# Kernel tuning notes

Measured on AMD Instinct MI355X. Metric: run time of the kernel, lower is better.

The kernel has to match this reference:

```python
import jax, jax.numpy as jnp
import numpy as np

B, D, H, W = 64, 64, 32, 32
K = 1024  # num_embeddings


def setup_inputs() -> dict:
    key = jax.random.key(0)
    kx, ke = jax.random.split(key)
    x = jax.random.normal(kx, (B, D, H, W), dtype=jnp.float32)
    # original init: uniform(-sqrt(3), sqrt(3)); randn is fine numerically, but
    # we match the original init distribution for fidelity
    limit = 3.0 ** 0.5
    embedding_table = jax.random.uniform(ke, (D, K), dtype=jnp.float32,
                                         minval=-limit, maxval=limit)
    return {"x": x, "embedding_table": embedding_table}


def reference(x, embedding_table):
    b, d, h, w = x.shape
    flat_x = x.transpose(0, 2, 3, 1).reshape(-1, d)            # [N, D]
    distances = ((flat_x ** 2).sum(1, keepdims=True)
                 - 2.0 * flat_x @ embedding_table
                 + (embedding_table ** 2).sum(0, keepdims=True))  # [N, K]
    encoding_indices = jnp.argmin(distances, axis=1)            # [N]
    quantized = embedding_table.T[encoding_indices]             # [N, D] gather
    quantized = quantized.reshape(b, h, w, d).transpose(0, 3, 1, 2)  # [B,D,H,W]
    dictionary_loss = jnp.mean((jax.lax.stop_gradient(x) - quantized) ** 2)
    commitment_loss = jnp.mean((x - jax.lax.stop_gradient(quantized)) ** 2)
    quantized_st = x + jax.lax.stop_gradient(quantized - x)     # straight-through
    return (quantized_st, dictionary_loss, commitment_loss,
            encoding_indices.reshape(b, -1))
```

## Files before the change

kernel.cpp:

```cpp
#include <hip/hip_runtime.h>


#define DDIM 64
#define KNUM 1024
#define HWN  1024
#define EPSS 0.01f

typedef __attribute__((ext_vector_type(8))) short short8v;
typedef __attribute__((ext_vector_type(4))) float f32x4;

__device__ __forceinline__ unsigned short bf16_rn(float v) {
    unsigned u = __float_as_uint(v);
    return (unsigned short)((u + 0x7FFFu + ((u >> 16) & 1u)) >> 16);
}
__device__ __forceinline__ float bf16f(unsigned short h) {
    return __uint_as_float(((unsigned)h) << 16);
}

__global__ __launch_bounds__(256) void vq_convert_e(const float* __restrict__ E,
                                                    float* __restrict__ esq,
                                                    unsigned short* __restrict__ eh,
                                                    unsigned short* __restrict__ el) {
    int k = blockIdx.x * 256 + threadIdx.x;
    float s = 0.f;
    #pragma unroll 8
    for (int d = 0; d < DDIM; ++d) {
        float v = E[d * KNUM + k];
        s = fmaf(v, v, s);
        unsigned short h = bf16_rn(v);
        float lo = v - bf16f(h);
        eh[k * DDIM + d] = h;
        el[k * DDIM + d] = bf16_rn(lo);
    }
    esq[k] = s;
}

__global__ __launch_bounds__(256, 4) void vq_mfma_fused(const float* __restrict__ x,
                                                        const float* __restrict__ E,
                                                        const unsigned short* __restrict__ eh,
                                                        const unsigned short* __restrict__ el,
                                                        const float* __restrict__ esq,
                                                        float* __restrict__ oidx,
                                                        float* __restrict__ out_q,
                                                        float* __restrict__ partial) {
    __shared__ unsigned short blds[2][8192];
    __shared__ float esqlds[KNUM];
    __shared__ int   klds[64];
    __shared__ float redlds[4];

    const int t = threadIdx.x;
    const int wv = t >> 6, l = t & 63;
    const int m = l & 15, g = l >> 4;
    const int tile = blockIdx.x * 4 + wv;
    const int n0 = blockIdx.x * 64;
    const int b  = n0 >> 10, hw0 = n0 & 1023;

    __builtin_amdgcn_global_load_lds(
        (const __attribute__((address_space(1))) void*)(esq + t * 4),
        (__attribute__((address_space(3))) void*)&esqlds[t * 4], 16, 0, 0);

    const int sr   = t >> 3;
    const int sc   = (t & 7) * 16;
    const int scsw = sc ^ ((sr & 7) << 4);
    const unsigned short* srcrow0 =
        (sr < 16) ? (eh + (size_t)sr * DDIM + (scsw >> 1))
                  : (el + (size_t)(sr - 16) * DDIM + (scsw >> 1));
    #define STAGEPH(BUF, P)                                                                  \
        _Pragma("unroll")                                                                    \
        for (int q = 0; q < 4; ++q)                                                          \
            __builtin_amdgcn_global_load_lds(                                                \
                (const __attribute__((address_space(1))) void*)(srcrow0 + (size_t)((P) * 4 + q) * 16 * DDIM), \
                (__attribute__((address_space(3))) void*)&blds[BUF][q * 2048 + t * 8],       \
                16, 0, 0);

    short8v axh[2], axl[2];
    {
        const int tn0 = tile * 16;
        const int tb = tn0 >> 10, thw = tn0 & 1023;
        const float* xg = x + (size_t)tb * (DDIM * HWN) + thw + m;
        #pragma unroll
        for (int s = 0; s < 2; ++s) {
            #pragma unroll
            for (int i = 0; i < 8; ++i) {
                float v = xg[(s * 32 + g * 8 + i) * HWN];
                unsigned short h = bf16_rn(v);
                axh[s][i] = (short)h;
                axl[s][i] = (short)bf16_rn(v - bf16f(h));
            }
        }
    }

    const int off_h0 = (m * 128 + (((g * 16)     ) ^ ((m & 7) << 4))) >> 1;
    const int off_h1 = (m * 128 + (((64 + g * 16)) ^ ((m & 7) << 4))) >> 1;
    const int off_l0 = off_h0 + 1024;
    const int off_l1 = off_h1 + 1024;

    float max1[4], max2[4]; int bk[4];
    #pragma unroll
    for (int j = 0; j < 4; ++j) { max1[j] = -3.4e38f; max2[j] = -3.4e38f; bk[j] = 0; }

    STAGEPH(0, 0);
    __syncthreads();

    for (int p = 0; p < 16; ++p) {
        const int cur = p & 1;
        if (p < 15) STAGEPH(cur ^ 1, p + 1);

        #pragma unroll
        for (int ktl = 0; ktl < 4; ++ktl) {
            const int kt = p * 4 + ktl;
            const unsigned short* bb = &blds[cur][ktl * 2048];
            const short8v bh0 = *reinterpret_cast<const short8v*>(bb + off_h0);
            const short8v bh1 = *reinterpret_cast<const short8v*>(bb + off_h1);
            const short8v bl0 = *reinterpret_cast<const short8v*>(bb + off_l0);
            const short8v bl1 = *reinterpret_cast<const short8v*>(bb + off_l1);
            const float ci = -0.5f * esqlds[kt * 16 + m];
            const f32x4 cinit = {ci, ci, ci, ci};

            f32x4 acc;
            acc = __builtin_amdgcn_mfma_f32_16x16x32_bf16(axh[0], bh0, cinit, 0, 0, 0);
            acc = __builtin_amdgcn_mfma_f32_16x16x32_bf16(axh[1], bh1, acc,  0, 0, 0);
            acc = __builtin_amdgcn_mfma_f32_16x16x32_bf16(axh[0], bl0, acc,  0, 0, 0);
            acc = __builtin_amdgcn_mfma_f32_16x16x32_bf16(axh[1], bl1, acc,  0, 0, 0);
            acc = __builtin_amdgcn_mfma_f32_16x16x32_bf16(axl[0], bh0, acc,  0, 0, 0);
            acc = __builtin_amdgcn_mfma_f32_16x16x32_bf16(axl[1], bh1, acc,  0, 0, 0);

            const int kcur = kt * 16 + m;
            #pragma unroll
            for (int j = 0; j < 4; ++j) {
                float s = acc[j];
                max2[j] = fmaxf(fminf(s, max1[j]), max2[j]);
                bool gt = s > max1[j];
                bk[j]   = gt ? kcur : bk[j];
                max1[j] = fmaxf(max1[j], s);
            }
        }
        __syncthreads();
    }
    #undef STAGEPH

    float* xlds = reinterpret_cast<float*>(&blds[0][0]);
    {
        const float* xbase = x + (size_t)b * (DDIM * HWN) + hw0;
        #pragma unroll
        for (int it = 0; it < 4; ++it) {
            int dbase = it * 16 + wv * 4;
            int dsub  = l >> 4;
            int off   = (l & 15) * 4;
            const float* gp = xbase + (dbase + dsub) * HWN + off;
            __builtin_amdgcn_global_load_lds(
                (const __attribute__((address_space(1))) void*)gp,
                (__attribute__((address_space(3))) void*)&xlds[dbase * 64 + l * 4],
                16, 0, 0);
        }
    }

    #pragma unroll
    for (int j = 0; j < 4; ++j) {
        float m1 = max1[j], m2 = max2[j]; int k1 = bk[j];
        #pragma unroll
        for (int off = 8; off >= 1; off >>= 1) {
            float om1 = __shfl_xor(m1, off, 16);
            float om2 = __shfl_xor(m2, off, 16);
            int   ok1 = __shfl_xor(k1, off, 16);
            if (om1 > m1 || (om1 == m1 && ok1 < k1)) {
                m2 = fmaxf(m1, om2); m1 = om1; k1 = ok1;
            } else {
                m2 = fmaxf(m2, (om1 == m1) ? om2 : om1);
            }
        }
        if (m == j) {
            int r = wv * 16 + g * 4 + j;
            klds[r] = (m1 - m2 < EPSS) ? -(k1 + 1) : k1;
        }
    }
    __syncthreads();

    for (int r = wv; r < 64; r += 4) {
        if (klds[r] >= 0) continue;
        float acc[16];
        #pragma unroll
        for (int kk = 0; kk < 16; ++kk) acc[kk] = 0.f;
        for (int d = 0; d < DDIM; ++d) {
            float xd = xlds[d * 64 + r];
            #pragma unroll
            for (int kk = 0; kk < 16; ++kk)
                acc[kk] = fmaf(xd, E[d * KNUM + kk * 64 + l], acc[kk]);
        }
        float bm = 3.4e38f; int bkk = KNUM;
        #pragma unroll
        for (int kk = 0; kk < 16; ++kk) {
            int k = kk * 64 + l;
            float dist = fmaf(-2.f, acc[kk], esqlds[k]);
            if (dist < bm) { bm = dist; bkk = k; }
        }
        #pragma unroll
        for (int off = 32; off >= 1; off >>= 1) {
            float ob = __shfl_xor(bm, off);
            int   ok = __shfl_xor(bkk, off);
            if (ob < bm || (ob == bm && ok < bkk)) { bm = ob; bkk = ok; }
        }
        if (l == 0) klds[r] = bkk;
    }
    __syncthreads();

    float lsum = 0.f;
    float* outbase = out_q + (size_t)b * (DDIM * HWN) + hw0;
    #pragma unroll 4
    for (int it = 0; it < 16; ++it) {
        int d = it * 4 + (t >> 6);
        int r = t & 63;
        int k = klds[r];
        float q  = E[d * KNUM + k];
        float xv = xlds[d * 64 + r];
        float diff = xv - q;
        lsum = fmaf(diff, diff, lsum);
        outbase[d * HWN + r] = q;
    }
    if (t < 64) oidx[n0 + t] = (float)klds[t];

    #pragma unroll
    for (int off = 32; off >= 1; off >>= 1)
        lsum += __shfl_xor(lsum, off);
    if ((t & 63) == 0) redlds[t >> 6] = lsum;
    __syncthreads();
    if (t == 0)
        partial[blockIdx.x] = (redlds[0] + redlds[1]) + (redlds[2] + redlds[3]);
}

__global__ __launch_bounds__(256) void vq_loss_kernel(const float* __restrict__ partial,
                                                      float* __restrict__ out_loss) {
    __shared__ float red[4];
    int t = threadIdx.x;
    float s = 0.f;
    #pragma unroll
    for (int it = 0; it < 4; ++it) s += partial[it * 256 + t];
    #pragma unroll
    for (int off = 32; off >= 1; off >>= 1) s += __shfl_xor(s, off);
    if ((t & 63) == 0) red[t >> 6] = s;
    __syncthreads();
    if (t == 0) {
        float loss = ((red[0] + red[1]) + (red[2] + red[3])) / 4194304.f;
        out_loss[0] = loss;
        out_loss[1] = loss;
    }
}

extern "C" void kernel_launch(void* const* d_in, const int* in_sizes, int n_in,
                              void* d_out, int out_size, void* d_ws, size_t ws_size,
                              hipStream_t stream) {
    const float* x = (const float*)d_in[0];
    const float* E = (const float*)d_in[1];
    float* out      = (float*)d_out;
    float* out_q    = out;
    float* out_loss = out + 4194304;
    float* oidx     = out + 4194306;

    float* esq     = (float*)d_ws;
    float* partial = esq + 1024;
    unsigned short* eh = (unsigned short*)(partial + 1024);
    unsigned short* el = eh + KNUM * DDIM;

    vq_convert_e<<<4, 256, 0, stream>>>(E, esq, eh, el);
    vq_mfma_fused<<<1024, 256, 0, stream>>>(x, E, eh, el, esq, oidx, out_q, partial);
    vq_loss_kernel<<<1, 256, 0, stream>>>(partial, out_loss);
}
```

Before: 64.07 us.

## Process two row tiles per wave to reuse staged codebook fragments

Each wave now computes two 16-row tiles against every staged codebook fragment, so a block covers 128 rows and the grid halves to 512 blocks. The LDS staging buffer doubles so each phase loads 8 k-tiles, halving the number of barrier phases. This cuts the codebook LDS traffic per row and the number of LDS reads per MFMA. The -0.5 scaling of the squared norms moves into the conversion kernel. In exchange it uses more registers and LDS, launch bounds drop to 2 blocks per CU, and fewer blocks means less parallelism across CUs.

Result: slower. 66.85 us (+4.3%).

```diff
diff --git a/kernel.cpp b/kernel.cpp
--- a/kernel.cpp
+++ b/kernel.cpp
@@ -18,7 +18,7 @@
 }
 
 __global__ __launch_bounds__(256) void vq_convert_e(const float* __restrict__ E,
-                                                    float* __restrict__ esq,
+                                                    float* __restrict__ esqm,
                                                     unsigned short* __restrict__ eh,
                                                     unsigned short* __restrict__ el) {
     int k = blockIdx.x * 256 + threadIdx.x;
@@ -32,32 +32,32 @@
         eh[k * DDIM + d] = h;
         el[k * DDIM + d] = bf16_rn(lo);
     }
-    esq[k] = s;
-}
-
-__global__ __launch_bounds__(256, 4) void vq_mfma_fused(const float* __restrict__ x,
+    esqm[k] = -0.5f * s;
+}
+
+__global__ __launch_bounds__(256, 2) void vq_mfma_fused(const float* __restrict__ x,
                                                         const float* __restrict__ E,
                                                         const unsigned short* __restrict__ eh,
                                                         const unsigned short* __restrict__ el,
-                                                        const float* __restrict__ esq,
+                                                        const float* __restrict__ esqm,
                                                         float* __restrict__ oidx,
                                                         float* __restrict__ out_q,
                                                         float* __restrict__ partial) {
-    __shared__ unsigned short blds[2][8192];
-    __shared__ float esqlds[KNUM];
-    __shared__ int   klds[64];
+    __shared__ unsigned short blds[2][16384];
+    __shared__ float esqmlds[KNUM];
+    __shared__ int   klds[128];
     __shared__ float redlds[4];
 
     const int t = threadIdx.x;
     const int wv = t >> 6, l = t & 63;
     const int m = l & 15, g = l >> 4;
-    const int tile = blockIdx.x * 4 + wv;
-    const int n0 = blockIdx.x * 64;
+    const int tileBase = blockIdx.x * 8 + wv * 2;
+    const int n0 = blockIdx.x * 128;
     const int b  = n0 >> 10, hw0 = n0 & 1023;
 
     __builtin_amdgcn_global_load_lds(
-        (const __attribute__((address_space(1))) void*)(esq + t * 4),
-        (__attribute__((address_space(3))) void*)&esqlds[t * 4], 16, 0, 0);
+        (const __attribute__((address_space(1))) void*)(esqm + t * 4),
+        (__attribute__((address_space(3))) void*)&esqmlds[t * 4], 16, 0, 0);
 
     const int sr   = t >> 3;
     const int sc   = (t & 7) * 16;
@@ -67,15 +67,16 @@
                   : (el + (size_t)(sr - 16) * DDIM + (scsw >> 1));
     #define STAGEPH(BUF, P)                                                                  \
         _Pragma("unroll")                                                                    \
-        for (int q = 0; q < 4; ++q)                                                          \
+        for (int q = 0; q < 8; ++q)                                                          \
             __builtin_amdgcn_global_load_lds(                                                \
-                (const __attribute__((address_space(1))) void*)(srcrow0 + (size_t)((P) * 4 + q) * 16 * DDIM), \
+                (const __attribute__((address_space(1))) void*)(srcrow0 + (size_t)((P) * 8 + q) * 16 * DDIM), \
                 (__attribute__((address_space(3))) void*)&blds[BUF][q * 2048 + t * 8],       \
                 16, 0, 0);
 
-    short8v axh[2], axl[2];
-    {
-        const int tn0 = tile * 16;
+    short8v axh[2][2], axl[2][2];
+    #pragma unroll
+    for (int T = 0; T < 2; ++T) {
+        const int tn0 = (tileBase + T) * 16;
         const int tb = tn0 >> 10, thw = tn0 & 1023;
         const float* xg = x + (size_t)tb * (DDIM * HWN) + thw + m;
         #pragma unroll
@@ -84,8 +85,8 @@
             for (int i = 0; i < 8; ++i) {
                 float v = xg[(s * 32 + g * 8 + i) * HWN];
                 unsigned short h = bf16_rn(v);
-                axh[s][i] = (short)h;
-                axl[s][i] = (short)bf16_rn(v - bf16f(h));
+                axh[T][s][i] = (short)h;
+                axl[T][s][i] = (short)bf16_rn(v - bf16f(h));
             }
         }
     }
@@ -95,44 +96,48 @@
     const int off_l0 = off_h0 + 1024;
     const int off_l1 = off_h1 + 1024;
 
-    float max1[4], max2[4]; int bk[4];
-    #pragma unroll
-    for (int j = 0; j < 4; ++j) { max1[j] = -3.4e38f; max2[j] = -3.4e38f; bk[j] = 0; }
+    float max1[2][4], max2[2][4]; int bk[2][4];
+    #pragma unroll
+    for (int T = 0; T < 2; ++T)
+        #pragma unroll
+        for (int j = 0; j < 4; ++j) { max1[T][j] = -3.4e38f; max2[T][j] = -3.4e38f; bk[T][j] = 0; }
 
     STAGEPH(0, 0);
     __syncthreads();
 
-    for (int p = 0; p < 16; ++p) {
+    for (int p = 0; p < 8; ++p) {
         const int cur = p & 1;
-        if (p < 15) STAGEPH(cur ^ 1, p + 1);
-
-        #pragma unroll
-        for (int ktl = 0; ktl < 4; ++ktl) {
-            const int kt = p * 4 + ktl;
+        if (p < 7) STAGEPH(cur ^ 1, p + 1);
+
+        #pragma unroll
+        for (int ktl = 0; ktl < 8; ++ktl) {
+            const int kt = p * 8 + ktl;
             const unsigned short* bb = &blds[cur][ktl * 2048];
             const short8v bh0 = *reinterpret_cast<const short8v*>(bb + off_h0);
             const short8v bh1 = *reinterpret_cast<const short8v*>(bb + off_h1);
             const short8v bl0 = *reinterpret_cast<const short8v*>(bb + off_l0);
             const short8v bl1 = *reinterpret_cast<const short8v*>(bb + off_l1);
-            const float ci = -0.5f * esqlds[kt * 16 + m];
+            const float ci = esqmlds[kt * 16 + m];
             const f32x4 cinit = {ci, ci, ci, ci};
-
-            f32x4 acc;
-            acc = __builtin_amdgcn_mfma_f32_16x16x32_bf16(axh[0], bh0, cinit, 0, 0, 0);
-            acc = __builtin_amdgcn_mfma_f32_16x16x32_bf16(axh[1], bh1, acc,  0, 0, 0);
-            acc = __builtin_amdgcn_mfma_f32_16x16x32_bf16(axh[0], bl0, acc,  0, 0, 0);
-            acc = __builtin_amdgcn_mfma_f32_16x16x32_bf16(axh[1], bl1, acc,  0, 0, 0);
-            acc = __builtin_amdgcn_mfma_f32_16x16x32_bf16(axl[0], bh0, acc,  0, 0, 0);
-            acc = __builtin_amdgcn_mfma_f32_16x16x32_bf16(axl[1], bh1, acc,  0, 0, 0);
-
             const int kcur = kt * 16 + m;
-            #pragma unroll
-            for (int j = 0; j < 4; ++j) {
-                float s = acc[j];
-                max2[j] = fmaxf(fminf(s, max1[j]), max2[j]);
-                bool gt = s > max1[j];
-                bk[j]   = gt ? kcur : bk[j];
-                max1[j] = fmaxf(max1[j], s);
+
+            #pragma unroll
+            for (int T = 0; T < 2; ++T) {
+                f32x4 acc;
+                acc = __builtin_amdgcn_mfma_f32_16x16x32_bf16(axh[T][0], bh0, cinit, 0, 0, 0);
+                acc = __builtin_amdgcn_mfma_f32_16x16x32_bf16(axh[T][1], bh1, acc,  0, 0, 0);
+                acc = __builtin_amdgcn_mfma_f32_16x16x32_bf16(axh[T][0], bl0, acc,  0, 0, 0);
+                acc = __builtin_amdgcn_mfma_f32_16x16x32_bf16(axh[T][1], bl1, acc,  0, 0, 0);
+                acc = __builtin_amdgcn_mfma_f32_16x16x32_bf16(axl[T][0], bh0, acc,  0, 0, 0);
+                acc = __builtin_amdgcn_mfma_f32_16x16x32_bf16(axl[T][1], bh1, acc,  0, 0, 0);
+                #pragma unroll
+                for (int j = 0; j < 4; ++j) {
+                    float s = acc[j];
+                    max2[T][j] = fmaxf(fminf(s, max1[T][j]), max2[T][j]);
+                    bool gt = s > max1[T][j];
+                    bk[T][j]   = gt ? kcur : bk[T][j];
+                    max1[T][j] = fmaxf(max1[T][j], s);
+                }
             }
         }
         __syncthreads();
@@ -143,62 +148,63 @@
     {
         const float* xbase = x + (size_t)b * (DDIM * HWN) + hw0;
         #pragma unroll
-        for (int it = 0; it < 4; ++it) {
-            int dbase = it * 16 + wv * 4;
-            int dsub  = l >> 4;
-            int off   = (l & 15) * 4;
-            const float* gp = xbase + (dbase + dsub) * HWN + off;
+        for (int it = 0; it < 8; ++it) {
+            int d   = it * 8 + (t >> 5);
+            int off = (t & 31) * 4;
+            const float* gp = xbase + d * HWN + off;
             __builtin_amdgcn_global_load_lds(
                 (const __attribute__((address_space(1))) void*)gp,
-                (__attribute__((address_space(3))) void*)&xlds[dbase * 64 + l * 4],
+                (__attribute__((address_space(3))) void*)&xlds[d * 128 + off],
                 16, 0, 0);
         }
     }
 
     #pragma unroll
-    for (int j = 0; j < 4; ++j) {
-        float m1 = max1[j], m2 = max2[j]; int k1 = bk[j];
-        #pragma unroll
-        for (int off = 8; off >= 1; off >>= 1) {
-            float om1 = __shfl_xor(m1, off, 16);
-            float om2 = __shfl_xor(m2, off, 16);
-            int   ok1 = __shfl_xor(k1, off, 16);
-            if (om1 > m1 || (om1 == m1 && ok1 < k1)) {
-                m2 = fmaxf(m1, om2); m1 = om1; k1 = ok1;
-            } else {
-                m2 = fmaxf(m2, (om1 == m1) ? om2 : om1);
-            }
-        }
-        if (m == j) {
-            int r = wv * 16 + g * 4 + j;
-            klds[r] = (m1 - m2 < EPSS) ? -(k1 + 1) : k1;
-        }
-    }
-    __syncthreads();
-
-    for (int r = wv; r < 64; r += 4) {
+    for (int T = 0; T < 2; ++T)
+        #pragma unroll
+        for (int j = 0; j < 4; ++j) {
+            float m1 = max1[T][j], m2 = max2[T][j]; int k1 = bk[T][j];
+            #pragma unroll
+            for (int off = 8; off >= 1; off >>= 1) {
+                float om1 = __shfl_xor(m1, off, 16);
+                float om2 = __shfl_xor(m2, off, 16);
+                int   ok1 = __shfl_xor(k1, off, 16);
+                if (om1 > m1 || (om1 == m1 && ok1 < k1)) {
+                    m2 = fmaxf(m1, om2); m1 = om1; k1 = ok1;
+                } else {
+                    m2 = fmaxf(m2, (om1 == m1) ? om2 : om1);
+                }
+            }
+            if (m == j) {
+                int r = (wv * 2 + T) * 16 + g * 4 + j;
+                klds[r] = (m1 - m2 < EPSS) ? -(k1 + 1) : k1;
+            }
+        }
+    __syncthreads();
+
+    for (int r = wv; r < 128; r += 4) {
         if (klds[r] >= 0) continue;
         float acc[16];
         #pragma unroll
         for (int kk = 0; kk < 16; ++kk) acc[kk] = 0.f;
         for (int d = 0; d < DDIM; ++d) {
-            float xd = xlds[d * 64 + r];
+            float xd = xlds[d * 128 + r];
             #pragma unroll
             for (int kk = 0; kk < 16; ++kk)
                 acc[kk] = fmaf(xd, E[d * KNUM + kk * 64 + l], acc[kk]);
         }
-        float bm = 3.4e38f; int bkk = KNUM;
+        float bm = -3.4e38f; int bkk = KNUM;
         #pragma unroll
         for (int kk = 0; kk < 16; ++kk) {
             int k = kk * 64 + l;
-            float dist = fmaf(-2.f, acc[kk], esqlds[k]);
-            if (dist < bm) { bm = dist; bkk = k; }
+            float sc = acc[kk] + esqmlds[k];
+            if (sc > bm) { bm = sc; bkk = k; }
         }
         #pragma unroll
         for (int off = 32; off >= 1; off >>= 1) {
             float ob = __shfl_xor(bm, off);
             int   ok = __shfl_xor(bkk, off);
-            if (ob < bm || (ob == bm && ok < bkk)) { bm = ob; bkk = ok; }
+            if (ob > bm || (ob == bm && ok < bkk)) { bm = ob; bkk = ok; }
         }
         if (l == 0) klds[r] = bkk;
     }
@@ -207,17 +213,18 @@
     float lsum = 0.f;
     float* outbase = out_q + (size_t)b * (DDIM * HWN) + hw0;
     #pragma unroll 4
-    for (int it = 0; it < 16; ++it) {
-        int d = it * 4 + (t >> 6);
-        int r = t & 63;
+    for (int it = 0; it < 32; ++it) {
+        int flat = it * 256 + t;
+        int d = flat >> 7;
+        int r = flat & 127;
         int k = klds[r];
         float q  = E[d * KNUM + k];
-        float xv = xlds[d * 64 + r];
+        float xv = xlds[d * 128 + r];
         float diff = xv - q;
         lsum = fmaf(diff, diff, lsum);
         outbase[d * HWN + r] = q;
     }
-    if (t < 64) oidx[n0 + t] = (float)klds[t];
+    if (t < 128) oidx[n0 + t] = (float)klds[t];
 
     #pragma unroll
     for (int off = 32; off >= 1; off >>= 1)
@@ -234,7 +241,7 @@
     int t = threadIdx.x;
     float s = 0.f;
     #pragma unroll
-    for (int it = 0; it < 4; ++it) s += partial[it * 256 + t];
+    for (int it = 0; it < 2; ++it) s += partial[it * 256 + t];
     #pragma unroll
     for (int off = 32; off >= 1; off >>= 1) s += __shfl_xor(s, off);
     if ((t & 63) == 0) red[t >> 6] = s;
@@ -256,12 +263,12 @@
     float* out_loss = out + 4194304;
     float* oidx     = out + 4194306;
 
-    float* esq     = (float*)d_ws;
-    float* partial = esq + 1024;
+    float* esqm    = (float*)d_ws;
+    float* partial = esqm + 1024;
     unsigned short* eh = (unsigned short*)(partial + 1024);
     unsigned short* el = eh + KNUM * DDIM;
 
-    vq_convert_e<<<4, 256, 0, stream>>>(E, esq, eh, el);
-    vq_mfma_fused<<<1024, 256, 0, stream>>>(x, E, eh, el, esq, oidx, out_q, partial);
+    vq_convert_e<<<4, 256, 0, stream>>>(E, esqm, eh, el);
+    vq_mfma_fused<<<512, 256, 0, stream>>>(x, E, eh, el, esqm, oidx, out_q, partial);
     vq_loss_kernel<<<1, 256, 0, stream>>>(partial, out_loss);
 }
```

## Split MFMA chain into independent accumulators and restructure LDS double-buffer sync

Applied to the files above, without the earlier changes.

The serial 6-MFMA dependency chain is replaced by three independent accumulator chains that are summed afterwards, which shortens MFMA latency stalls. The -0.5*|e|^2 term is precomputed in the conversion kernel, and the exact rescoring pass is rewritten to maximize that score instead of minimizing distance. The per-stage __syncthreads is replaced by explicit s_barrier plus vmcnt waits, so the prefetch of the next stage can stay in flight. The runner-up tracking in the shuffle reduction is also simplified, which slightly changes the near-tie detection and adds a few extra adds per tile.

Result: slower. 67.42 us (+5.2%).

```diff
diff --git a/kernel.cpp b/kernel.cpp
--- a/kernel.cpp
+++ b/kernel.cpp
@@ -9,6 +9,9 @@
 typedef __attribute__((ext_vector_type(8))) short short8v;
 typedef __attribute__((ext_vector_type(4))) float f32x4;
 
+#define VMWAIT(N) do { asm volatile("s_waitcnt vmcnt(" #N ")" ::: "memory"); \
+                       __builtin_amdgcn_sched_barrier(0); } while (0)
+
 __device__ __forceinline__ unsigned short bf16_rn(float v) {
     unsigned u = __float_as_uint(v);
     return (unsigned short)((u + 0x7FFFu + ((u >> 16) & 1u)) >> 16);
@@ -18,7 +21,7 @@
 }
 
 __global__ __launch_bounds__(256) void vq_convert_e(const float* __restrict__ E,
-                                                    float* __restrict__ esq,
+                                                    float* __restrict__ esqm,
                                                     unsigned short* __restrict__ eh,
                                                     unsigned short* __restrict__ el) {
     int k = blockIdx.x * 256 + threadIdx.x;
@@ -32,19 +35,19 @@
         eh[k * DDIM + d] = h;
         el[k * DDIM + d] = bf16_rn(lo);
     }
-    esq[k] = s;
+    esqm[k] = -0.5f * s;
 }
 
 __global__ __launch_bounds__(256, 4) void vq_mfma_fused(const float* __restrict__ x,
                                                         const float* __restrict__ E,
                                                         const unsigned short* __restrict__ eh,
                                                         const unsigned short* __restrict__ el,
-                                                        const float* __restrict__ esq,
+                                                        const float* __restrict__ esqm,
                                                         float* __restrict__ oidx,
                                                         float* __restrict__ out_q,
                                                         float* __restrict__ partial) {
     __shared__ unsigned short blds[2][8192];
-    __shared__ float esqlds[KNUM];
+    __shared__ float esqmlds[KNUM];
     __shared__ int   klds[64];
     __shared__ float redlds[4];
 
@@ -56,8 +59,8 @@
     const int b  = n0 >> 10, hw0 = n0 & 1023;
 
     __builtin_amdgcn_global_load_lds(
-        (const __attribute__((address_space(1))) void*)(esq + t * 4),
-        (__attribute__((address_space(3))) void*)&esqlds[t * 4], 16, 0, 0);
+        (const __attribute__((address_space(1))) void*)(esqm + t * 4),
+        (__attribute__((address_space(3))) void*)&esqmlds[t * 4], 16, 0, 0);
 
     const int sr   = t >> 3;
     const int sc   = (t & 7) * 16;
@@ -99,12 +102,16 @@
     #pragma unroll
     for (int j = 0; j < 4; ++j) { max1[j] = -3.4e38f; max2[j] = -3.4e38f; bk[j] = 0; }
 
+    const f32x4 zf = {0.f, 0.f, 0.f, 0.f};
+
     STAGEPH(0, 0);
-    __syncthreads();
 
     for (int p = 0; p < 16; ++p) {
         const int cur = p & 1;
-        if (p < 15) STAGEPH(cur ^ 1, p + 1);
+        __builtin_amdgcn_s_barrier();
+        if (p < 15) { STAGEPH(cur ^ 1, p + 1); VMWAIT(4); }
+        else        { VMWAIT(0); }
+        __builtin_amdgcn_s_barrier();
 
         #pragma unroll
         for (int ktl = 0; ktl < 4; ++ktl) {
@@ -114,30 +121,30 @@
             const short8v bh1 = *reinterpret_cast<const short8v*>(bb + off_h1);
             const short8v bl0 = *reinterpret_cast<const short8v*>(bb + off_l0);
             const short8v bl1 = *reinterpret_cast<const short8v*>(bb + off_l1);
-            const float ci = -0.5f * esqlds[kt * 16 + m];
-            const f32x4 cinit = {ci, ci, ci, ci};
-
-            f32x4 acc;
-            acc = __builtin_amdgcn_mfma_f32_16x16x32_bf16(axh[0], bh0, cinit, 0, 0, 0);
-            acc = __builtin_amdgcn_mfma_f32_16x16x32_bf16(axh[1], bh1, acc,  0, 0, 0);
-            acc = __builtin_amdgcn_mfma_f32_16x16x32_bf16(axh[0], bl0, acc,  0, 0, 0);
-            acc = __builtin_amdgcn_mfma_f32_16x16x32_bf16(axh[1], bl1, acc,  0, 0, 0);
-            acc = __builtin_amdgcn_mfma_f32_16x16x32_bf16(axl[0], bh0, acc,  0, 0, 0);
-            acc = __builtin_amdgcn_mfma_f32_16x16x32_bf16(axl[1], bh1, acc,  0, 0, 0);
-
+            const float ci = esqmlds[kt * 16 + m];
             const int kcur = kt * 16 + m;
+
+            f32x4 a0, a1, a2;
+            a0 = __builtin_amdgcn_mfma_f32_16x16x32_bf16(axh[0], bh0, zf, 0, 0, 0);
+            a1 = __builtin_amdgcn_mfma_f32_16x16x32_bf16(axh[0], bl0, zf, 0, 0, 0);
+            a2 = __builtin_amdgcn_mfma_f32_16x16x32_bf16(axl[0], bh0, zf, 0, 0, 0);
+            a0 = __builtin_amdgcn_mfma_f32_16x16x32_bf16(axh[1], bh1, a0, 0, 0, 0);
+            a1 = __builtin_amdgcn_mfma_f32_16x16x32_bf16(axh[1], bl1, a1, 0, 0, 0);
+            a2 = __builtin_amdgcn_mfma_f32_16x16x32_bf16(axl[1], bh1, a2, 0, 0, 0);
+
             #pragma unroll
             for (int j = 0; j < 4; ++j) {
-                float s = acc[j];
+                float s = (a0[j] + a1[j]) + (a2[j] + ci);
                 max2[j] = fmaxf(fminf(s, max1[j]), max2[j]);
                 bool gt = s > max1[j];
                 bk[j]   = gt ? kcur : bk[j];
                 max1[j] = fmaxf(max1[j], s);
             }
         }
-        __syncthreads();
     }
     #undef STAGEPH
+
+    __syncthreads();
 
     float* xlds = reinterpret_cast<float*>(&blds[0][0]);
     {
@@ -166,7 +173,7 @@
             if (om1 > m1 || (om1 == m1 && ok1 < k1)) {
                 m2 = fmaxf(m1, om2); m1 = om1; k1 = ok1;
             } else {
-                m2 = fmaxf(m2, (om1 == m1) ? om2 : om1);
+                m2 = fmaxf(m2, om1);
             }
         }
         if (m == j) {
@@ -187,18 +194,18 @@
             for (int kk = 0; kk < 16; ++kk)
                 acc[kk] = fmaf(xd, E[d * KNUM + kk * 64 + l], acc[kk]);
         }
-        float bm = 3.4e38f; int bkk = KNUM;
+        float bm = -3.4e38f; int bkk = KNUM;
         #pragma unroll
         for (int kk = 0; kk < 16; ++kk) {
             int k = kk * 64 + l;
-            float dist = fmaf(-2.f, acc[kk], esqlds[k]);
-            if (dist < bm) { bm = dist; bkk = k; }
+            float sc = acc[kk] + esqmlds[k];
+            if (sc > bm) { bm = sc; bkk = k; }
         }
         #pragma unroll
         for (int off = 32; off >= 1; off >>= 1) {
             float ob = __shfl_xor(bm, off);
             int   ok = __shfl_xor(bkk, off);
-            if (ob < bm || (ob == bm && ok < bkk)) { bm = ob; bkk = ok; }
+            if (ob > bm || (ob == bm && ok < bkk)) { bm = ob; bkk = ok; }
         }
         if (l == 0) klds[r] = bkk;
     }
@@ -256,12 +263,12 @@
     float* out_loss = out + 4194304;
     float* oidx     = out + 4194306;
 
-    float* esq     = (float*)d_ws;
-    float* partial = esq + 1024;
+    float* esqm    = (float*)d_ws;
+    float* partial = esqm + 1024;
     unsigned short* eh = (unsigned short*)(partial + 1024);
     unsigned short* el = eh + KNUM * DDIM;
 
-    vq_convert_e<<<4, 256, 0, stream>>>(E, esq, eh, el);
-    vq_mfma_fused<<<1024, 256, 0, stream>>>(x, E, eh, el, esq, oidx, out_q, partial);
+    vq_convert_e<<<4, 256, 0, stream>>>(E, esqm, eh, el);
+    vq_mfma_fused<<<1024, 256, 0, stream>>>(x, E, eh, el, esqm, oidx, out_q, partial);
     vq_loss_kernel<<<1, 256, 0, stream>>>(partial, out_loss);
 }
```
